# Kernel tuning notes

Measured on AMD Instinct MI355X. Metric: run time of the kernel, lower is better.

Reference implementation:

```python
import jax, jax.numpy as jnp
import numpy as np

SIGMA = 1.0  # RBF kernel bandwidth (init kwarg)

def setup_inputs() -> dict:
    key = jax.random.key(0)
    ks = jax.random.split(key, 5)
    B, N, D_in, D_emb = 8, 2048, 1024, 512
    scale = 1.0 / np.sqrt(D_in)
    return {
        "x": jax.random.normal(ks[0], (B, N, D_in), jnp.float32),
        "W_mu": jax.random.normal(ks[1], (D_emb, D_in), jnp.float32) * scale,
        "b_mu": jax.random.normal(ks[2], (D_emb,), jnp.float32) * scale,
        "W_logvar": jax.random.normal(ks[3], (D_emb, D_in), jnp.float32) * scale,
        "b_logvar": jax.random.normal(ks[4], (D_emb,), jnp.float32) * scale,
    }

def reference(x, W_mu, b_mu, W_logvar, b_logvar):
    # dual linear heads: (B,N,D_in) -> (B,N,D_emb)
    mu = jnp.einsum('bnd,ed->bne', x, W_mu) + b_mu
    logvar = jnp.einsum('bnd,ed->bne', x, W_logvar) + b_logvar
    sigma = jnp.exp(0.5 * logvar)
    # RBF kernel matrix K(x, x): (B,N,N) via ||xi||^2 + ||xj||^2 - 2 xi.xj
    sq = jnp.sum(x * x, axis=-1)                       # (B,N)
    gram = jnp.einsum('bnd,bmd->bnm', x, x)            # (B,N,N)
    dist = sq[:, :, None] + sq[:, None, :] - 2.0 * gram
    K = jnp.exp(-dist / (2.0 * SIGMA ** 2))            # (B,N,N)
    cov_diag = jnp.diagonal(K, axis1=1, axis2=2)       # (B,N) == exp(0) = 1
    sigma_adjusted = sigma * cov_diag[..., None]       # (B,N,D_emb)
    return (mu, sigma_adjusted)
```

## Files before the change

kernel.cpp:

```cpp
#include <hip/hip_runtime.h>
#include <hip/hip_bf16.h>
#include <math.h>

typedef __bf16 bf16;
typedef __attribute__((ext_vector_type(4))) float f32x4;
typedef __attribute__((ext_vector_type(4))) bf16 bf16x4;
typedef __attribute__((ext_vector_type(8))) bf16 bf16x8;

#define M_TOT 16384
#define K_TOT 1024
#define D_EMB 512
#define NT 32

__global__ __launch_bounds__(256) void cvt_w_img(
    const float* __restrict__ W_mu, const float* __restrict__ W_logvar,
    bf16* __restrict__ img)
{
    const int c  = blockIdx.x * 256 + threadIdx.x;
    const int l  = c & 63;
    const int kt = (c >> 6) & 31;
    const int es = c >> 11;
    const int col = es * 16 + (l & 15);
    const int k0  = kt * 32 + (l >> 4) * 8;
    const float* s = (col < D_EMB) ? (W_mu + (size_t)col * K_TOT + k0)
                                   : (W_logvar + (size_t)(col - D_EMB) * K_TOT + k0);
    f32x4 a = ((const f32x4*)s)[0];
    f32x4 b = ((const f32x4*)s)[1];
    bf16x8 o;
    o[0] = (bf16)a[0]; o[1] = (bf16)a[1]; o[2] = (bf16)a[2]; o[3] = (bf16)a[3];
    o[4] = (bf16)b[0]; o[5] = (bf16)b[1]; o[6] = (bf16)b[2]; o[7] = (bf16)b[3];
    *(bf16x8*)(img + (size_t)c * 8) = o;
}

__global__ __launch_bounds__(512, 1) void gpe_tall2(
    const float* __restrict__ x,
    const bf16* __restrict__ wimg,
    const float* __restrict__ b_mu,
    const float* __restrict__ b_logvar,
    float* __restrict__ out)
{
    __shared__ __align__(16) bf16 Alds[64 * 1024];

    const int tid  = threadIdx.x;
    const int lane = tid & 63;
    const int wc   = tid >> 6;
    const int fr   = lane & 15;
    const int g16  = lane >> 4;
    const int frx  = fr & 7;
    const int bm   = blockIdx.x;

    const bf16* __restrict__ bb = wimg + (size_t)(wc * 8) * (NT * 512) + lane * 8;

    bf16x8 bvA[8], bvB[8];
    auto loadB = [&](int t, bf16x8 (&bv)[8]) {
#pragma unroll
        for (int ns = 0; ns < 8; ++ns)
            bv[ns] = *(const bf16x8*)(bb + (size_t)ns * (NT * 512) + t * 512);
    };

    loadB(0, bvA);
    loadB(1, bvB);

    {
        const int arow = tid >> 3;
        const int sl0  = tid & 7;
        const float* __restrict__ Asrc = x + (size_t)(bm * 64 + arow) * K_TOT;
        const int rx = arow & 7;
#pragma unroll
        for (int j = 0; j < 16; ++j) {
            const int slot = sl0 + 8 * j;
            f32x4 a = *(const f32x4*)(Asrc + slot * 8);
            f32x4 b = *(const f32x4*)(Asrc + slot * 8 + 4);
            bf16x8 w;
#pragma unroll
            for (int q = 0; q < 4; ++q) { w[q] = (bf16)a[q]; w[q + 4] = (bf16)b[q]; }
            *(bf16x8*)&Alds[arow * 1024 + (slot ^ rx) * 8] = w;
        }
    }
    __syncthreads();

    f32x4 acc[4][8];
#pragma unroll
    for (int m = 0; m < 4; ++m)
#pragma unroll
        for (int n = 0; n < 8; ++n)
            acc[m][n] = (f32x4){0.f, 0.f, 0.f, 0.f};

#define TILE_BODY(T, BVC)                                                      \
    {                                                                          \
        const int t = (T);                                                     \
        bf16x8 afc[4];                                                         \
        _Pragma("unroll")                                                      \
        for (int m = 0; m < 4; ++m)                                            \
            afc[m] = *(const bf16x8*)&Alds[(m * 16 + fr) * 1024                \
                                           + ((t * 4 + g16) ^ frx) * 8];       \
        __builtin_amdgcn_s_setprio(1);                                         \
        _Pragma("unroll")                                                      \
        for (int ns = 0; ns < 8; ++ns)                                         \
            _Pragma("unroll")                                                  \
            for (int m = 0; m < 4; ++m)                                        \
                acc[m][ns] = __builtin_amdgcn_mfma_f32_16x16x32_bf16(          \
                    afc[m], BVC[ns], acc[m][ns], 0, 0, 0);                     \
        __builtin_amdgcn_s_setprio(0);                                         \
        if (t + 2 < NT) loadB(t + 2, BVC);     \
    }

    for (int t0 = 0; t0 < NT; t0 += 2) {
        TILE_BODY(t0,     bvA)
        TILE_BODY(t0 + 1, bvB)
    }
#undef TILE_BODY

    const bool is_mu = (wc < 4);
    const float* __restrict__ bias = is_mu ? b_mu : b_logvar;
    float* __restrict__ obase = is_mu ? out : (out + (size_t)M_TOT * D_EMB);
    const int clbase = (wc & 3) * 128;

#pragma unroll
    for (int m = 0; m < 4; ++m) {
        const int row0 = bm * 64 + m * 16 + g16 * 4;
#pragma unroll
        for (int ns = 0; ns < 8; ++ns) {
            const int cl = clbase + ns * 16 + fr;
            const float bvs = bias[cl];
#pragma unroll
            for (int j = 0; j < 4; ++j) {
                float v = acc[m][ns][j] + bvs;
                if (!is_mu) v = __expf(0.5f * v);
                obase[(size_t)(row0 + j) * D_EMB + cl] = v;
            }
        }
    }
}

#define LDS_STRIDE 40
__global__ __launch_bounds__(256) void gpe_gemm_fb(
    const float* __restrict__ x, const float* __restrict__ W_mu,
    const float* __restrict__ b_mu, const float* __restrict__ W_logvar,
    const float* __restrict__ b_logvar, float* __restrict__ out)
{
    __shared__ __align__(16) bf16 As[128][LDS_STRIDE];
    __shared__ __align__(16) bf16 Bs[128][LDS_STRIDE];
    const int tid = threadIdx.x, lane = tid & 63, wid = tid >> 6;
    const int wr = wid >> 1, wcn = wid & 1;
    const int bn = blockIdx.x & 7, bm = blockIdx.x >> 3;
    const int ebase = bn * 128;
    const bool is_mu = (ebase < D_EMB);
    const float* Wp = is_mu ? (W_mu + (size_t)ebase * K_TOT)
                            : (W_logvar + (size_t)(ebase - D_EMB) * K_TOT);
    const float* bias = is_mu ? b_mu : b_logvar;
    const int cbase = is_mu ? ebase : (ebase - D_EMB);
    float* obase = is_mu ? out : (out + (size_t)M_TOT * D_EMB);
    const float* Ap = x + (size_t)(bm * 128) * K_TOT;
    f32x4 acc[4][4];
#pragma unroll
    for (int m = 0; m < 4; ++m)
#pragma unroll
        for (int n = 0; n < 4; ++n) acc[m][n] = (f32x4){0.f, 0.f, 0.f, 0.f};
    const int fr = lane & 15, fk = (lane >> 4) * 8;
    const int arow = wr * 64 + fr, brow = wcn * 64 + fr;
    for (int kt = 0; kt < K_TOT / 32; ++kt) {
        const int k0 = kt * 32;
#pragma unroll
        for (int s = 0; s < 4; ++s) {
            const int idx = s * 256 + tid;
            const int row = idx >> 3, col = (idx & 7) << 2;
            f32x4 va = *reinterpret_cast<const f32x4*>(Ap + (size_t)row * K_TOT + k0 + col);
            f32x4 vb = *reinterpret_cast<const f32x4*>(Wp + (size_t)row * K_TOT + k0 + col);
            bf16x4 ha, hb;
#pragma unroll
            for (int j = 0; j < 4; ++j) { ha[j] = (bf16)va[j]; hb[j] = (bf16)vb[j]; }
            *reinterpret_cast<bf16x4*>(&As[row][col]) = ha;
            *reinterpret_cast<bf16x4*>(&Bs[row][col]) = hb;
        }
        __syncthreads();
        bf16x8 af[4], bfv[4];
#pragma unroll
        for (int m = 0; m < 4; ++m)
            af[m] = *reinterpret_cast<const bf16x8*>(&As[arow + m * 16][fk]);
#pragma unroll
        for (int n = 0; n < 4; ++n)
            bfv[n] = *reinterpret_cast<const bf16x8*>(&Bs[brow + n * 16][fk]);
#pragma unroll
        for (int m = 0; m < 4; ++m)
#pragma unroll
            for (int n = 0; n < 4; ++n)
                acc[m][n] = __builtin_amdgcn_mfma_f32_16x16x32_bf16(af[m], bfv[n], acc[m][n], 0, 0, 0);
        __syncthreads();
    }
#pragma unroll
    for (int m = 0; m < 4; ++m) {
        const int rbase = bm * 128 + wr * 64 + m * 16 + (lane >> 4) * 4;
#pragma unroll
        for (int n = 0; n < 4; ++n) {
            const int c = cbase + wcn * 64 + n * 16 + (lane & 15);
            const float bv = bias[c];
#pragma unroll
            for (int j = 0; j < 4; ++j) {
                float v = acc[m][n][j] + bv;
                if (!is_mu) v = __expf(0.5f * v);
                obase[(size_t)(rbase + j) * D_EMB + c] = v;
            }
        }
    }
}

extern "C" void kernel_launch(void* const* d_in, const int* in_sizes, int n_in,
                              void* d_out, int out_size, void* d_ws, size_t ws_size,
                              hipStream_t stream) {
    const float* x        = (const float*)d_in[0];
    const float* W_mu     = (const float*)d_in[1];
    const float* b_mu     = (const float*)d_in[2];
    const float* W_logvar = (const float*)d_in[3];
    const float* b_logvar = (const float*)d_in[4];
    float* out = (float*)d_out;

    const size_t ws_needed = (size_t)1024 * 1024 * sizeof(bf16);

    if (ws_size >= ws_needed) {
        bf16* wimg = (bf16*)d_ws;
        cvt_w_img<<<512, 256, 0, stream>>>(W_mu, W_logvar, wimg);
        gpe_tall2<<<256, 512, 0, stream>>>(x, wimg, b_mu, b_logvar, out);
    } else {
        gpe_gemm_fb<<<1024, 256, 0, stream>>>(x, W_mu, b_mu, W_logvar, b_logvar, out);
    }
}
```

Before: 53.72 us.

## Pipeline A-tile staging with MFMA and split output into two column passes

The kernel now loads and converts the x tile into LDS in four chunks, overlapping the global loads of later chunks with MFMA work on earlier ones instead of staging the whole tile before any compute. Each wave now computes 64 columns per pass and makes two passes, mu then logvar, which halves the live accumulator and B-register count. The mu results are stored while the B operands for the logvar pass are prefetched. This trades one larger GEMM phase for two sequential passes that both re-read the LDS A tile, with the goal of hiding the A-load latency and easing register pressure.

```diff
diff --git a/kernel.cpp b/kernel.cpp
--- a/kernel.cpp
+++ b/kernel.cpp
@@ -32,7 +32,7 @@
     *(bf16x8*)(img + (size_t)c * 8) = o;
 }
 
-__global__ __launch_bounds__(512, 1) void gpe_tall2(
+__global__ __launch_bounds__(512, 1) void gpe_tall3(
     const float* __restrict__ x,
     const bf16* __restrict__ wimg,
     const float* __restrict__ b_mu,
@@ -49,44 +49,53 @@
     const int frx  = fr & 7;
     const int bm   = blockIdx.x;
 
-    const bf16* __restrict__ bb = wimg + (size_t)(wc * 8) * (NT * 512) + lane * 8;
-
-    bf16x8 bvA[8], bvB[8];
-    auto loadB = [&](int t, bf16x8 (&bv)[8]) {
-#pragma unroll
-        for (int ns = 0; ns < 8; ++ns)
-            bv[ns] = *(const bf16x8*)(bb + (size_t)ns * (NT * 512) + t * 512);
+    const int arow = tid >> 3;
+    const int sl0  = tid & 7;
+    const int rx   = arow & 7;
+    const float* __restrict__ Asrc = x + (size_t)(bm * 64 + arow) * K_TOT;
+
+    f32x4 stg[8];
+    auto gload = [&](int c) {
+#pragma unroll
+        for (int j = 0; j < 4; ++j) {
+            const int s = c * 32 + sl0 + 8 * j;
+            stg[2 * j]     = *(const f32x4*)(Asrc + s * 8);
+            stg[2 * j + 1] = *(const f32x4*)(Asrc + s * 8 + 4);
+        }
     };
-
-    loadB(0, bvA);
-    loadB(1, bvB);
-
-    {
-        const int arow = tid >> 3;
-        const int sl0  = tid & 7;
-        const float* __restrict__ Asrc = x + (size_t)(bm * 64 + arow) * K_TOT;
-        const int rx = arow & 7;
-#pragma unroll
-        for (int j = 0; j < 16; ++j) {
-            const int slot = sl0 + 8 * j;
-            f32x4 a = *(const f32x4*)(Asrc + slot * 8);
-            f32x4 b = *(const f32x4*)(Asrc + slot * 8 + 4);
+    auto cvtwrite = [&](int c) {
+#pragma unroll
+        for (int j = 0; j < 4; ++j) {
+            const int s = c * 32 + sl0 + 8 * j;
             bf16x8 w;
 #pragma unroll
-            for (int q = 0; q < 4; ++q) { w[q] = (bf16)a[q]; w[q + 4] = (bf16)b[q]; }
-            *(bf16x8*)&Alds[arow * 1024 + (slot ^ rx) * 8] = w;
-        }
-    }
-    __syncthreads();
-
-    f32x4 acc[4][8];
+            for (int q = 0; q < 4; ++q) {
+                w[q]     = (bf16)stg[2 * j][q];
+                w[q + 4] = (bf16)stg[2 * j + 1][q];
+            }
+            *(bf16x8*)&Alds[arow * 1024 + (s ^ rx) * 8] = w;
+        }
+    };
+
+    const bf16* __restrict__ bl = wimg + lane * 8;
+    bf16x8 bvA[4], bvB[4];
+    auto loadB = [&](size_t e0, int t, bf16x8 (&bv)[4]) {
+#pragma unroll
+        for (int ns = 0; ns < 4; ++ns)
+            bv[ns] = *(const bf16x8*)(bl + e0 + (size_t)ns * 16384 + t * 512);
+    };
+
+    f32x4 acc[4][4];
 #pragma unroll
     for (int m = 0; m < 4; ++m)
 #pragma unroll
-        for (int n = 0; n < 8; ++n)
+        for (int n = 0; n < 4; ++n)
             acc[m][n] = (f32x4){0.f, 0.f, 0.f, 0.f};
 
-#define TILE_BODY(T, BVC)                                                      \
+    const size_t e0p0 = (size_t)(wc * 4) * 16384;
+    const size_t e0p1 = (size_t)(32 + wc * 4) * 16384;
+
+#define TILE_BODY(T, E0, BVC)                                                  \
     {                                                                          \
         const int t = (T);                                                     \
         bf16x8 afc[4];                                                         \
@@ -96,38 +105,75 @@
                                            + ((t * 4 + g16) ^ frx) * 8];       \
         __builtin_amdgcn_s_setprio(1);                                         \
         _Pragma("unroll")                                                      \
-        for (int ns = 0; ns < 8; ++ns)                                         \
+        for (int ns = 0; ns < 4; ++ns)                                         \
             _Pragma("unroll")                                                  \
             for (int m = 0; m < 4; ++m)                                        \
                 acc[m][ns] = __builtin_amdgcn_mfma_f32_16x16x32_bf16(          \
                     afc[m], BVC[ns], acc[m][ns], 0, 0, 0);                     \
         __builtin_amdgcn_s_setprio(0);                                         \
-        if (t + 2 < NT) loadB(t + 2, BVC);     \
-    }
-
-    for (int t0 = 0; t0 < NT; t0 += 2) {
-        TILE_BODY(t0,     bvA)
-        TILE_BODY(t0 + 1, bvB)
+        if (t + 2 < NT) loadB(E0, t + 2, BVC);                                 \
+    }
+
+    gload(0);
+    for (int c = 0; c < 4; ++c) {
+        if (c == 0) asm volatile("s_waitcnt vmcnt(0)" ::: "memory");
+        else        asm volatile("s_waitcnt vmcnt(8)" ::: "memory");
+        cvtwrite(c);
+        if (c < 3) gload(c + 1);
+        if (c == 0) { loadB(e0p0, 0, bvA); loadB(e0p0, 1, bvB); }
+        asm volatile("s_waitcnt lgkmcnt(0)" ::: "memory");
+        __builtin_amdgcn_s_barrier();
+#pragma unroll
+        for (int tt = 0; tt < 8; tt += 2) {
+            TILE_BODY(c * 8 + tt,     e0p0, bvA)
+            TILE_BODY(c * 8 + tt + 1, e0p0, bvB)
+        }
+    }
+
+    loadB(e0p1, 0, bvA);
+    loadB(e0p1, 1, bvB);
+    {
+        float* __restrict__ obase = out;
+#pragma unroll
+        for (int m = 0; m < 4; ++m) {
+            const int row0 = bm * 64 + m * 16 + g16 * 4;
+#pragma unroll
+            for (int ns = 0; ns < 4; ++ns) {
+                const int cl = wc * 64 + ns * 16 + fr;
+                const float bvs = b_mu[cl];
+#pragma unroll
+                for (int j = 0; j < 4; ++j)
+                    obase[(size_t)(row0 + j) * D_EMB + cl] = acc[m][ns][j] + bvs;
+            }
+        }
+    }
+
+#pragma unroll
+    for (int m = 0; m < 4; ++m)
+#pragma unroll
+        for (int n = 0; n < 4; ++n)
+            acc[m][n] = (f32x4){0.f, 0.f, 0.f, 0.f};
+
+#pragma unroll
+    for (int tt = 0; tt < NT; tt += 2) {
+        TILE_BODY(tt,     e0p1, bvA)
+        TILE_BODY(tt + 1, e0p1, bvB)
     }
 #undef TILE_BODY
 
-    const bool is_mu = (wc < 4);
-    const float* __restrict__ bias = is_mu ? b_mu : b_logvar;
-    float* __restrict__ obase = is_mu ? out : (out + (size_t)M_TOT * D_EMB);
-    const int clbase = (wc & 3) * 128;
-
-#pragma unroll
-    for (int m = 0; m < 4; ++m) {
-        const int row0 = bm * 64 + m * 16 + g16 * 4;
-#pragma unroll
-        for (int ns = 0; ns < 8; ++ns) {
-            const int cl = clbase + ns * 16 + fr;
-            const float bvs = bias[cl];
-#pragma unroll
-            for (int j = 0; j < 4; ++j) {
-                float v = acc[m][ns][j] + bvs;
-                if (!is_mu) v = __expf(0.5f * v);
-                obase[(size_t)(row0 + j) * D_EMB + cl] = v;
+    {
+        float* __restrict__ obase = out + (size_t)M_TOT * D_EMB;
+#pragma unroll
+        for (int m = 0; m < 4; ++m) {
+            const int row0 = bm * 64 + m * 16 + g16 * 4;
+#pragma unroll
+            for (int ns = 0; ns < 4; ++ns) {
+                const int cl = wc * 64 + ns * 16 + fr;
+                const float bvs = b_logvar[cl];
+#pragma unroll
+                for (int j = 0; j < 4; ++j)
+                    obase[(size_t)(row0 + j) * D_EMB + cl] =
+                        __expf(0.5f * (acc[m][ns][j] + bvs));
             }
         }
     }
@@ -220,7 +266,7 @@
     if (ws_size >= ws_needed) {
         bf16* wimg = (bf16*)d_ws;
         cvt_w_img<<<512, 256, 0, stream>>>(W_mu, W_logvar, wimg);
-        gpe_tall2<<<256, 512, 0, stream>>>(x, wimg, b_mu, b_logvar, out);
+        gpe_tall3<<<256, 512, 0, stream>>>(x, wimg, b_mu, b_logvar, out);
     } else {
         gpe_gemm_fb<<<1024, 256, 0, stream>>>(x, W_mu, b_mu, W_logvar, b_logvar, out);
     }
```

Result: faster. 48.58 us, median of 4 (-9.6%).
